# Kernel tuning notes

Hardware: AMD Instinct MI355X
Metric: run time of the kernel (lower is better)

The kernel has to match this reference:

```python
import jax, jax.numpy as jnp
import numpy as np
from jax import lax


def conv2d(x, w, b, pad):
    out = lax.conv_general_dilated(x, w, (1, 1), [(pad, pad), (pad, pad)],
                                   dimension_numbers=('NCHW', 'OIHW', 'NCHW'))
    return out + b[None, :, None, None]


def deform_conv3x3(src, offset, weight, bias):
    # torchvision.ops.deform_conv2d, 3x3 kernel, stride 1, pad 1, no mask.
    # src [B,C,H,W]; offset [B,18,H,W] laid out (y,x) per kernel pos, row-major.
    B, C, H, W = src.shape
    off = offset.reshape(B, 9, 2, H, W)
    ky, kx = jnp.meshgrid(jnp.arange(3) - 1, jnp.arange(3) - 1, indexing='ij')
    ky = ky.reshape(9).astype(src.dtype)
    kx = kx.reshape(9).astype(src.dtype)
    yy = jnp.arange(H, dtype=src.dtype)[:, None]
    xx = jnp.arange(W, dtype=src.dtype)[None, :]
    py = yy[None, None] + ky[None, :, None, None] + off[:, :, 0]  # [B,9,H,W]
    px = xx[None, None] + kx[None, :, None, None] + off[:, :, 1]
    y0 = jnp.floor(py)
    x0 = jnp.floor(px)
    wy1 = py - y0
    wx1 = px - x0

    def gather(yi, xi):
        valid = ((yi >= 0) & (yi < H) & (xi >= 0) & (xi < W)).astype(src.dtype)
        yc = jnp.clip(yi, 0, H - 1).astype(jnp.int32)
        xc = jnp.clip(xi, 0, W - 1).astype(jnp.int32)
        vals = jax.vmap(lambda s, a, c: s[:, a, c])(src, yc, xc)  # [B,C,9,H,W]
        return vals * valid[:, None]

    sampled = (gather(y0, x0) * ((1 - wy1) * (1 - wx1))[:, None]
               + gather(y0, x0 + 1) * ((1 - wy1) * wx1)[:, None]
               + gather(y0 + 1, x0) * (wy1 * (1 - wx1))[:, None]
               + gather(y0 + 1, x0 + 1) * (wy1 * wx1)[:, None])
    wk = weight.reshape(weight.shape[0], weight.shape[1], 9)
    return jnp.einsum('bckhw,ock->bohw', sampled, wk) + bias[None, :, None, None]


def setup_inputs() -> dict:
    key = jax.random.key(0)
    ks = jax.random.split(key, 16)
    B, C, H, W, N = 1, 256, 96, 96, 8
    current_feat = jax.random.normal(ks[0], (B, C, H, W), dtype=jnp.float32)
    neighbor_feats = jax.random.normal(ks[1], (N, B, C, H, W), dtype=jnp.float32)
    coord_diffs = jax.random.normal(ks[2], (N, 4), dtype=jnp.float32)
    align_w = jax.random.normal(ks[3], (C, C, 3, 3), dtype=jnp.float32) * 0.02
    align_b = jax.random.normal(ks[4], (C,), dtype=jnp.float32) * 0.02
    offset_w = jax.random.normal(ks[5], (18, 2 * C, 3, 3), dtype=jnp.float32) * 0.002
    offset_b = jax.random.normal(ks[6], (18,), dtype=jnp.float32) * 0.002
    gate1_w = jax.random.normal(ks[7], (C // 2, 2 * C, 3, 3), dtype=jnp.float32) * 0.02
    gate1_b = jax.random.normal(ks[8], (C // 2,), dtype=jnp.float32) * 0.02
    gate2_w = jax.random.normal(ks[9], (1, C // 2, 1, 1), dtype=jnp.float32) * 0.02
    gate2_b = jax.random.normal(ks[10], (1,), dtype=jnp.float32) * 0.02
    enc_w = jax.random.normal(ks[11], (C, 4), dtype=jnp.float32) * 0.1
    enc_b = jax.random.normal(ks[12], (C,), dtype=jnp.float32) * 0.1
    return dict(current_feat=current_feat, neighbor_feats=neighbor_feats,
                coord_diffs=coord_diffs, align_w=align_w, align_b=align_b,
                offset_w=offset_w, offset_b=offset_b, gate1_w=gate1_w,
                gate1_b=gate1_b, gate2_w=gate2_w, gate2_b=gate2_b,
                enc_w=enc_w, enc_b=enc_b)


def reference(current_feat, neighbor_feats, coord_diffs, align_w, align_b,
              offset_w, offset_b, gate1_w, gate1_b, gate2_w, gate2_b,
              enc_w, enc_b):
    B, C, H, W = current_feat.shape
    N = neighbor_feats.shape[0]
    aligned = []
    for n in range(N):  # fixed small neighbor set (<= 8)
        src = neighbor_feats[n]
        concat = jnp.concatenate([src, current_feat], axis=1)  # [B,2C,H,W]
        offset = conv2d(concat, offset_w, offset_b, 1)         # [B,18,H,W]
        aligned.append(deform_conv3x3(src, offset, align_w, align_b))
    all_feats = jnp.stack(aligned, axis=1)                     # [B,N,C,H,W]
    # coordinate embedding: Linear(4 -> C) per neighbor, shaped [1,N,C,1,1]
    coord_embs = (coord_diffs @ enc_w.T + enc_b)[None, :, :, None, None]
    cur_exp = jnp.broadcast_to(current_feat[:, None], (B, N, C, H, W))
    energy = jnp.concatenate([cur_exp, all_feats], axis=2).reshape(B * N, 2 * C, H, W)
    g = jax.nn.relu(conv2d(energy, gate1_w, gate1_b, 1))
    g = jax.nn.sigmoid(conv2d(g, gate2_w, gate2_b, 0))          # [B*N,1,H,W]
    weights = jax.nn.softmax(g.reshape(B, N, 1, H, W), axis=1)
    fused = (all_feats * weights + coord_embs).sum(axis=1)      # [B,C,H,W]
    return current_feat + 0.5 * fused
```

## Files before the change

### kernel.cpp

```cpp
#include <hip/hip_runtime.h>
#include <math.h>

#define CH   256
#define HH   96
#define WW   96
#define NN   8
#define HWSZ 9216
#define PLANE (HWSZ*CH)

typedef unsigned short u16;
typedef unsigned int   u32;
typedef short bf16x8 __attribute__((ext_vector_type(8)));
typedef float f32x4  __attribute__((ext_vector_type(4)));
typedef float f32x2  __attribute__((ext_vector_type(2)));

__device__ inline u16 f2bf(float f) {
    union { float f; u32 u; } v; v.f = f;
    u32 r = v.u + 0x7FFF + ((v.u >> 16) & 1);
    return (u16)(r >> 16);
}
__device__ inline float bflo(u32 u) {
    union { u32 u; float f; } v; v.u = u << 16; return v.f;
}
__device__ inline float bfhi(u32 u) {
    union { u32 u; float f; } v; v.u = u & 0xffff0000u; return v.f;
}
__device__ inline u32 pk2bf(float lo, float hi) {
    union { float f; u32 u; } a, b; a.f = lo; b.f = hi;
    u32 ra = a.u + 0x7FFF + ((a.u >> 16) & 1);
    u32 rb = b.u + 0x7FFF + ((b.u >> 16) & 1);
    return (ra >> 16) | (rb & 0xffff0000u);
}

__global__ void k_emb_sum(const float* __restrict__ cd,
                          const float* __restrict__ enc_w,
                          const float* __restrict__ enc_b,
                          float* __restrict__ emb)
{
    int c = threadIdx.x;
    float s = 0.f;
    for (int n = 0; n < NN; ++n) {
        float d = enc_b[c];
        #pragma unroll
        for (int j = 0; j < 4; ++j) d += cd[n*4 + j] * enc_w[c*4 + j];
        s += d;
    }
    emb[c] = s;
}

__global__ __launch_bounds__(256) void k_to_nhwc(const float* __restrict__ in,
                                                 u16* __restrict__ out)
{
    int n = blockIdx.y;
    int p0 = blockIdx.x * 64;
    int tid = threadIdx.x;
    __shared__ u16 T[64][262];

    int px4 = (tid & 15) * 4, cb = tid >> 4;
    for (int it = 0; it < 16; ++it) {
        int c = cb + it*16;
        float4 v = *reinterpret_cast<const float4*>(
            in + ((size_t)n*CH + c)*HWSZ + p0 + px4);
        T[px4+0][c] = f2bf(v.x);
        T[px4+1][c] = f2bf(v.y);
        T[px4+2][c] = f2bf(v.z);
        T[px4+3][c] = f2bf(v.w);
    }
    __syncthreads();
    int pxb = tid >> 5, ck = tid & 31;
    for (int it = 0; it < 8; ++it) {
        int p = pxb + it*8;
        *reinterpret_cast<int4*>(out + (size_t)n*PLANE + (size_t)(p0+p)*CH + ck*8) =
            *reinterpret_cast<const int4*>(&T[p][ck*8]);
    }
}

__global__ void k_pack_w(const float* __restrict__ w, u16* __restrict__ wp,
                         int O, int O_pad, int CIN)
{
    int idx = blockIdx.x * 256 + threadIdx.x;
    int total = O_pad * CIN * 9;
    if (idx >= total) return;
    int o = idx / (CIN * 9);
    int K = idx % (CIN * 9);
    int tap = K / CIN, c = K % CIN;
    float v = (o < O) ? w[((size_t)o * CIN + c) * 9 + tap] : 0.f;
    int NKC = (CIN * 9) >> 5;
    int kc = K >> 5, kl = K & 31;
    int lane = (kl >> 3) * 16 + (o & 15);
    size_t dstp = (((size_t)(o >> 4) * NKC + kc) * 64 + lane) * 8 + (kl & 7);
    wp[dstp] = f2bf(v);
}

template<int MTW, int EPI>
__global__ __launch_bounds__(512) void k_conv_nhwc(
    const u16* __restrict__ in0, long s0,
    const u16* __restrict__ in1, long s1,
    const u16* __restrict__ Wp, const float* __restrict__ b1,
    const float* __restrict__ g2w, const float* __restrict__ g2b,
    float* __restrict__ out)
{
    constexpr int NKC = 144, NCC = 16;
    int n = blockIdx.x, t = blockIdx.y;
    int tx0 = (t % 3) * 32, ty0 = (t / 3) * 8;
    int tid = threadIdx.x, lane = tid & 63, w = tid >> 6;
    int mh = w >> 2, pg = w & 3;
    int colq = lane >> 4;

    __shared__ __align__(16) u16 SB[340*40];
    __shared__ float gpart[8][64];

    f32x4 acc[MTW][4];
    #pragma unroll
    for (int mt = 0; mt < MTW; ++mt)
        #pragma unroll
        for (int nf = 0; nf < 4; ++nf)
            acc[mt][nf] = (f32x4){0.f,0.f,0.f,0.f};

    int bidx[4];
    #pragma unroll
    for (int nf = 0; nf < 4; ++nf) {
        int px = pg*64 + nf*16 + (lane & 15);
        int row = px >> 5, col = px & 31;
        bidx[nf] = ((row+1)*34 + (col+1))*40 + colq*8;
    }

    for (int cc = 0; cc < NCC; ++cc) {
        const u16* base = (cc < 8) ? in0 + (size_t)n*s0 + cc*32
                                   : in1 + (size_t)n*s1 + (cc-8)*32;
        for (int i = tid; i < 1360; i += 512) {
            int ph = i >> 2, q = i & 3;
            int r = ph / 34, col = ph - r*34;
            int y = ty0 - 1 + r, x = tx0 - 1 + col;
            bool v = ((unsigned)y < (unsigned)HH) && ((unsigned)x < (unsigned)WW);
            int off = v ? (y*WW + x)*CH : 0;
            int4 val = *reinterpret_cast<const int4*>(base + off + q*8);
            if (!v) val = make_int4(0,0,0,0);
            *reinterpret_cast<int4*>(&SB[ph*40 + q*8]) = val;
        }
        __syncthreads();
        #pragma unroll
        for (int tap = 0; tap < 9; ++tap) {
            int kc = tap*NCC + cc;
            bf16x8 a[MTW];
            #pragma unroll
            for (int mt = 0; mt < MTW; ++mt)
                a[mt] = *reinterpret_cast<const bf16x8*>(
                    Wp + (((size_t)(mh*MTW+mt)*NKC + kc)*64 + lane)*8);
            const int dy = tap/3 - 1, dx = tap%3 - 1;
            #pragma unroll
            for (int nf = 0; nf < 4; ++nf) {
                bf16x8 b = *reinterpret_cast<const bf16x8*>(
                    &SB[bidx[nf] + (dy*34 + dx)*40]);
                #pragma unroll
                for (int mt = 0; mt < MTW; ++mt)
                    acc[mt][nf] = __builtin_amdgcn_mfma_f32_16x16x32_bf16(
                                      a[mt], b, acc[mt][nf], 0, 0, 0);
            }
        }
        __syncthreads();
    }

    if (EPI == 0) {
        #pragma unroll
        for (int nf = 0; nf < 4; ++nf) {
            int px = pg*64 + nf*16 + (lane & 15);
            int gp = (ty0 + (px>>5))*WW + tx0 + (px & 31);
            #pragma unroll
            for (int mt = 0; mt < MTW; ++mt) {
                int o_base = (mh*MTW+mt)*16 + colq*4;
                #pragma unroll
                for (int r = 0; r < 4; ++r) {
                    int o = o_base + r;
                    if (o < 18)
                        out[((size_t)n*18 + o)*HWSZ + gp] = acc[mt][nf][r] + b1[o];
                }
            }
        }
    } else {
        float part[4];
        #pragma unroll
        for (int nf = 0; nf < 4; ++nf) {
            float s = 0.f;
            #pragma unroll
            for (int mt = 0; mt < MTW; ++mt) {
                int o_base = (mh*MTW+mt)*16 + colq*4;
                #pragma unroll
                for (int r = 0; r < 4; ++r) {
                    int o = o_base + r;
                    float vv = fmaxf(acc[mt][nf][r] + b1[o], 0.f);
                    s += vv * g2w[o];
                }
            }
            part[nf] = s;
        }
        #pragma unroll
        for (int nf = 0; nf < 4; ++nf) {
            part[nf] += __shfl_xor(part[nf], 16, 64);
            part[nf] += __shfl_xor(part[nf], 32, 64);
        }
        if (lane < 16) {
            #pragma unroll
            for (int nf = 0; nf < 4; ++nf)
                gpart[w][nf*16 + lane] = part[nf];
        }
        __syncthreads();
        if (tid < 256) {
            int pxl = tid & 63, pgg = tid >> 6;
            float s = gpart[pgg][pxl] + gpart[4 + pgg][pxl] + g2b[0];
            float g = 1.f / (1.f + expf(-s));
            int px = pgg*64 + pxl;
            int gp = (ty0 + (px>>5))*WW + tx0 + (px & 31);
            out[(size_t)n*HWSZ + gp] = g;
        }
    }
}

__global__ __launch_bounds__(256) void k_deform_nhwc(
    const u16* __restrict__ nbrh, const float* __restrict__ offs,
    const u16* __restrict__ Wp, const float* __restrict__ ab,
    u16* __restrict__ alig)
{
    constexpr int NKC = 72;
    int n = blockIdx.x, t = blockIdx.y;
    int tx0 = (t % 3) * 32, ty0 = (t / 3) * 2;
    int tid = threadIdx.x, lane = tid & 63, w = tid >> 6;
    int colq = lane >> 4;

    __shared__ __align__(16) char pool[26624];
    u16*    SB0  = (u16*)pool;
    u16*    SB1  = SB0 + 2048;
    int4*   cofs = (int4*)(pool + 8192);
    float4* cwt  = (float4*)(pool + 17408);

    const u16* src = nbrh + (size_t)n * PLANE;

    for (int i = tid; i < 576; i += 256) {
        int tt = i >> 6, p = i & 63;
        int y = ty0 + (p>>5), x = tx0 + (p & 31);
        int pp = y*WW + x;
        float oy = offs[((size_t)n*18 + 2*tt    )*HWSZ + pp];
        float ox = offs[((size_t)n*18 + 2*tt + 1)*HWSZ + pp];
        float py  = (float)y + (float)(tt/3 - 1) + oy;
        float pxx = (float)x + (float)(tt%3 - 1) + ox;
        py  = fminf(fmaxf(py,  -4.f), 100.f);
        pxx = fminf(fmaxf(pxx, -4.f), 100.f);
        float y0f = floorf(py), x0f = floorf(pxx);
        int y0 = (int)y0f, x0 = (int)x0f;
        float wy = py - y0f, wx = pxx - x0f;
        bool b00 = (y0 >= 0)  & (y0 < HH)   & (x0 >= 0)  & (x0 < WW);
        bool b01 = (y0 >= 0)  & (y0 < HH)   & (x0 >= -1) & (x0 < WW-1);
        bool b10 = (y0 >= -1) & (y0 < HH-1) & (x0 >= 0)  & (x0 < WW);
        bool b11 = (y0 >= -1) & (y0 < HH-1) & (x0 >= -1) & (x0 < WW-1);
        int a00 = (y0*WW + x0)*CH;
        int4 o4;
        o4.x = b00 ? a00             : 0;
        o4.y = b01 ? a00 + CH        : 0;
        o4.z = b10 ? a00 + WW*CH     : 0;
        o4.w = b11 ? a00 + WW*CH+CH  : 0;
        float4 w4;
        w4.x = b00 ? (1.f-wy)*(1.f-wx) : 0.f;
        w4.y = b01 ? (1.f-wy)*wx       : 0.f;
        w4.z = b10 ? wy*(1.f-wx)       : 0.f;
        w4.w = b11 ? wy*wx             : 0.f;
        cofs[i] = o4; cwt[i] = w4;
    }
    __syncthreads();

    f32x4 acc[4][4];
    #pragma unroll
    for (int mt = 0; mt < 4; ++mt)
        #pragma unroll
        for (int nf = 0; nf < 4; ++nf)
            acc[mt][nf] = (f32x4){0.f,0.f,0.f,0.f};

    int sbw = ((lane>>4)*4 + w)*128 + (lane&15)*8;
    int bb[4];
    #pragma unroll
    for (int nf = 0; nf < 4; ++nf)
        bb[nf] = (nf*4 + colq)*128 + (lane&15)*8;

    int4 o4; float4 w4;
    int4 crn[4];
    bf16x8 apf[4];

    auto loadC = [&](int kc) {
        int c0 = (kc & 7)*32 + w*8;
        crn[0] = *reinterpret_cast<const int4*>(src + o4.x + c0);
        crn[1] = *reinterpret_cast<const int4*>(src + o4.y + c0);
        crn[2] = *reinterpret_cast<const int4*>(src + o4.z + c0);
        crn[3] = *reinterpret_cast<const int4*>(src + o4.w + c0);
    };
    auto loadA = [&](int kc) {
        #pragma unroll
        for (int mt = 0; mt < 4; ++mt)
            apf[mt] = *reinterpret_cast<const bf16x8*>(
                Wp + (((size_t)(w*4+mt)*NKC + kc)*64 + lane)*8);
    };
    auto bilerp = [&](float4 wt, const int4* q) -> int4 {
        f32x2 W00 = {wt.x, wt.x}, W01 = {wt.y, wt.y};
        f32x2 W10 = {wt.z, wt.z}, W11 = {wt.w, wt.w};
        int4 res;
        #pragma unroll
        for (int j = 0; j < 4; ++j) {
            u32 u00 = ((const u32*)&q[0])[j], u01 = ((const u32*)&q[1])[j];
            u32 u10 = ((const u32*)&q[2])[j], u11 = ((const u32*)&q[3])[j];
            f32x2 c00 = {bflo(u00), bfhi(u00)};
            f32x2 c01 = {bflo(u01), bfhi(u01)};
            f32x2 c10 = {bflo(u10), bfhi(u10)};
            f32x2 c11 = {bflo(u11), bfhi(u11)};
            f32x2 v = c00*W00;
            v += c01*W01;
            v += c10*W10;
            v += c11*W11;
            ((u32*)&res)[j] = pk2bf(v.x, v.y);
        }
        return res;
    };

    o4 = cofs[lane]; w4 = cwt[lane];
    loadC(0);
    loadA(0);
    int cur = 0;
    for (int kc = 0; kc < NKC; ++kc) {
        int4 vpk = bilerp(w4, crn);
        u16* SBc = cur ? SB1 : SB0;
        *reinterpret_cast<int4*>(&SBc[sbw]) = vpk;
        bf16x8 a4[4];
        #pragma unroll
        for (int mt = 0; mt < 4; ++mt) a4[mt] = apf[mt];
        int kn = kc + 1;
        if (kn < NKC) {
            if ((kn & 7) == 0) {
                int r = (kn >> 3)*64 + lane;
                o4 = cofs[r]; w4 = cwt[r];
            }
            loadC(kn);
            loadA(kn);
        }
        __syncthreads();
        #pragma unroll
        for (int nf = 0; nf < 4; ++nf) {
            bf16x8 b = *reinterpret_cast<const bf16x8*>(&SBc[bb[nf]]);
            #pragma unroll
            for (int mt = 0; mt < 4; ++mt)
                acc[mt][nf] = __builtin_amdgcn_mfma_f32_16x16x32_bf16(
                                  a4[mt], b, acc[mt][nf], 0, 0, 0);
        }
        cur ^= 1;
    }

    __syncthreads();
    u16* TO = (u16*)pool;
    u16* aligp = alig + (size_t)n * PLANE;
    #pragma unroll
    for (int h = 0; h < 2; ++h) {
        #pragma unroll
        for (int sub = 0; sub < 2; ++sub) {
            int nf = 2*h + sub;
            int pl = sub*16 + (lane & 15);
            #pragma unroll
            for (int mt = 0; mt < 4; ++mt) {
                int o = (w*4+mt)*16 + colq*4;
                ushort4 v;
                v.x = f2bf(acc[mt][nf][0] + ab[o]);
                v.y = f2bf(acc[mt][nf][1] + ab[o+1]);
                v.z = f2bf(acc[mt][nf][2] + ab[o+2]);
                v.w = f2bf(acc[mt][nf][3] + ab[o+3]);
                *reinterpret_cast<ushort4*>(&TO[pl*264 + o]) = v;
            }
        }
        __syncthreads();
        #pragma unroll
        for (int it = 0; it < 4; ++it) {
            int i = tid + it*256;
            int pr = i >> 5, ck = i & 31;
            int nf = 2*h + (pr >> 4);
            int pxx = nf*16 + (pr & 15);
            int gp = (ty0 + (pxx>>5))*WW + tx0 + (pxx & 31);
            *reinterpret_cast<int4*>(aligp + (size_t)gp*CH + ck*8) =
                *reinterpret_cast<const int4*>(&TO[pr*264 + ck*8]);
        }
        __syncthreads();
    }
}

__global__ __launch_bounds__(256) void k_fuse_nhwc(
    const float* __restrict__ cur, const u16* __restrict__ alig,
    const float* __restrict__ g, const float* __restrict__ emb,
    float* __restrict__ out)
{
    int p0 = blockIdx.x * 32;
    int tid = threadIdx.x;
    __shared__ float wE[NN][32];
    __shared__ float trans[256][33];

    if (tid < 32) {
        int p = p0 + tid;
        float e[NN], m = -1e30f;
        #pragma unroll
        for (int n = 0; n < NN; ++n) { e[n] = g[n*HWSZ + p]; m = fmaxf(m, e[n]); }
        float se = 0.f;
        #pragma unroll
        for (int n = 0; n < NN; ++n) { e[n] = expf(e[n] - m); se += e[n]; }
        float inv = 1.f / se;
        #pragma unroll
        for (int n = 0; n < NN; ++n) wE[n][tid] = e[n] * inv;
    }
    __syncthreads();

    #pragma unroll
    for (int it = 0; it < 4; ++it) {
        int i = tid + it*256;
        int px = i >> 5, ck = i & 31;
        float a8[8];
        #pragma unroll
        for (int j = 0; j < 8; ++j) a8[j] = 0.f;
        #pragma unroll
        for (int n = 0; n < NN; ++n) {
            int4 v = *reinterpret_cast<const int4*>(
                &alig[((size_t)n*HWSZ + p0 + px)*CH + ck*8]);
            float f = wE[n][px];
            #pragma unroll
            for (int j4 = 0; j4 < 4; ++j4) {
                u32 u = ((const u32*)&v)[j4];
                a8[2*j4]   += bflo(u) * f;
                a8[2*j4+1] += bfhi(u) * f;
            }
        }
        #pragma unroll
        for (int j = 0; j < 8; ++j) {
            int c = ck*8 + j;
            trans[c][px ^ (c & 31)] = a8[j] + emb[c];
        }
    }
    __syncthreads();
    for (int it = 0; it < 32; ++it) {
        int c = (tid >> 5) + it*8, px = tid & 31;
        int idx = c*HWSZ + p0 + px;
        out[idx] = cur[idx] + 0.5f * trans[c][px ^ (c & 31)];
    }
}

extern "C" void kernel_launch(void* const* d_in, const int* in_sizes, int n_in,
                              void* d_out, int out_size, void* d_ws, size_t ws_size,
                              hipStream_t stream)
{
    const float* cur = (const float*)d_in[0];
    const float* nbr = (const float*)d_in[1];
    const float* cd  = (const float*)d_in[2];
    const float* aw  = (const float*)d_in[3];
    const float* ab  = (const float*)d_in[4];
    const float* ow  = (const float*)d_in[5];
    const float* ob  = (const float*)d_in[6];
    const float* g1w = (const float*)d_in[7];
    const float* g1b = (const float*)d_in[8];
    const float* g2w = (const float*)d_in[9];
    const float* g2b = (const float*)d_in[10];
    const float* ew  = (const float*)d_in[11];
    const float* eb  = (const float*)d_in[12];
    float* out = (float*)d_out;
    float* ws  = (float*)d_ws;

    float* offs = ws;
    float* gbuf = offs + 1327104;
    float* emb  = gbuf + 73728;
    u16* nbrh = (u16*)(emb + 256);
    u16* curh = nbrh + (size_t)NN*PLANE;
    u16* alig = curh + PLANE;
    u16* wpO  = alig + (size_t)NN*PLANE;
    u16* wpG  = wpO + 147456;
    u16* wpA  = wpG + 589824;

    k_emb_sum<<<dim3(1), dim3(256), 0, stream>>>(cd, ew, eb, emb);
    k_to_nhwc<<<dim3(144, 8), dim3(256), 0, stream>>>(nbr, nbrh);
    k_to_nhwc<<<dim3(144, 1), dim3(256), 0, stream>>>(cur, curh);
    k_pack_w<<<dim3((32*4608 + 255)/256), dim3(256), 0, stream>>>(ow, wpO, 18, 32, 512);
    k_pack_w<<<dim3((128*4608 + 255)/256), dim3(256), 0, stream>>>(g1w, wpG, 128, 128, 512);
    k_pack_w<<<dim3((256*2304 + 255)/256), dim3(256), 0, stream>>>(aw, wpA, 256, 256, 256);

    k_conv_nhwc<1, 0><<<dim3(8, 36), dim3(512), 0, stream>>>(
        nbrh, (long)PLANE, curh, 0L, wpO, ob, nullptr, nullptr, offs);
    k_deform_nhwc<<<dim3(8, 144), dim3(256), 0, stream>>>(nbrh, offs, wpA, ab, alig);
    k_conv_nhwc<4, 1><<<dim3(8, 36), dim3(512), 0, stream>>>(
        curh, 0L, alig, (long)PLANE, wpG, g1b, g2w, g2b, gbuf);
    k_fuse_nhwc<<<dim3(288), dim3(256), 0, stream>>>(cur, alig, gbuf, emb, out);
}
```

Baseline: 435.0 us.

## Prefetch two K-chunks ahead and remap gather threads with swizzled LDS layout

```diff
diff --git a/kernel.cpp b/kernel.cpp
--- a/kernel.cpp
+++ b/kernel.cpp
@@ -274,24 +274,30 @@
         for (int nf = 0; nf < 4; ++nf)
             acc[mt][nf] = (f32x4){0.f,0.f,0.f,0.f};
 
-    int sbw = ((lane>>4)*4 + w)*128 + (lane&15)*8;
+    int px = tid >> 2, chq = tid & 3;
+    int sbw = ((px>>4)*4 + chq)*128 + (((px&15) ^ (chq<<2)))*8;
     int bb[4];
     #pragma unroll
     for (int nf = 0; nf < 4; ++nf)
-        bb[nf] = (nf*4 + colq)*128 + (lane&15)*8;
-
-    int4 o4; float4 w4;
-    int4 crn[4];
-    bf16x8 apf[4];
-
-    auto loadC = [&](int kc) {
-        int c0 = (kc & 7)*32 + w*8;
+        bb[nf] = (nf*4 + colq)*128 + (((lane&15) ^ (colq<<2)))*8;
+    int c0base = chq*8;
+
+    int4 o4_0, o4_1; float4 w4_0, w4_1;
+    int4 crn0[4], crn1[4];
+    bf16x8 apf0[4], apf1[4];
+
+    auto loadCoord = [&](int kc, int4& o4, float4& w4) {
+        int r = (kc >> 3)*64 + px;
+        o4 = cofs[r]; w4 = cwt[r];
+    };
+    auto loadC = [&](int kc, const int4& o4, int4* crn) {
+        int c0 = (kc & 7)*32 + c0base;
         crn[0] = *reinterpret_cast<const int4*>(src + o4.x + c0);
         crn[1] = *reinterpret_cast<const int4*>(src + o4.y + c0);
         crn[2] = *reinterpret_cast<const int4*>(src + o4.z + c0);
         crn[3] = *reinterpret_cast<const int4*>(src + o4.w + c0);
     };
-    auto loadA = [&](int kc) {
+    auto loadA = [&](int kc, bf16x8* apf) {
         #pragma unroll
         for (int mt = 0; mt < 4; ++mt)
             apf[mt] = *reinterpret_cast<const bf16x8*>(
@@ -318,25 +324,19 @@
         return res;
     };
 
-    o4 = cofs[lane]; w4 = cwt[lane];
-    loadC(0);
-    loadA(0);
     int cur = 0;
-    for (int kc = 0; kc < NKC; ++kc) {
+    auto step = [&](int kc, int4& o4, float4& w4, int4* crn, bf16x8* apf) {
         int4 vpk = bilerp(w4, crn);
         u16* SBc = cur ? SB1 : SB0;
         *reinterpret_cast<int4*>(&SBc[sbw]) = vpk;
         bf16x8 a4[4];
         #pragma unroll
         for (int mt = 0; mt < 4; ++mt) a4[mt] = apf[mt];
-        int kn = kc + 1;
+        int kn = kc + 2;
         if (kn < NKC) {
-            if ((kn & 7) == 0) {
-                int r = (kn >> 3)*64 + lane;
-                o4 = cofs[r]; w4 = cwt[r];
-            }
-            loadC(kn);
-            loadA(kn);
+            if ((kn & 7) < 2) loadCoord(kn, o4, w4);
+            loadC(kn, o4, crn);
+            loadA(kn, apf);
         }
         __syncthreads();
         #pragma unroll
@@ -348,6 +348,16 @@
                                   a4[mt], b, acc[mt][nf], 0, 0, 0);
         }
         cur ^= 1;
+    };
+
+    loadCoord(0, o4_0, w4_0);
+    loadCoord(1, o4_1, w4_1);
+    loadC(0, o4_0, crn0); loadA(0, apf0);
+    loadC(1, o4_1, crn1); loadA(1, apf1);
+
+    for (int kc = 0; kc < NKC; kc += 2) {
+        step(kc,     o4_0, w4_0, crn0, apf0);
+        step(kc + 1, o4_1, w4_1, crn1, apf1);
     }
 
     __syncthreads();
```

New measurement: 406.8 us. 6.5% less time.

## Warp-specialize deform conv into bilinear producer and MFMA consumer waves

Applied to the files above, without the earlier changes.

```diff
diff --git a/kernel.cpp b/kernel.cpp
--- a/kernel.cpp
+++ b/kernel.cpp
@@ -216,7 +216,7 @@
     }
 }
 
-__global__ __launch_bounds__(256) void k_deform_nhwc(
+__global__ __launch_bounds__(512, 4) void k_deform_nhwc(
     const u16* __restrict__ nbrh, const float* __restrict__ offs,
     const u16* __restrict__ Wp, const float* __restrict__ ab,
     u16* __restrict__ alig)
@@ -227,15 +227,15 @@
     int tid = threadIdx.x, lane = tid & 63, w = tid >> 6;
     int colq = lane >> 4;
 
-    __shared__ __align__(16) char pool[26624];
+    __shared__ __align__(16) char pool[29696];
     u16*    SB0  = (u16*)pool;
-    u16*    SB1  = SB0 + 2048;
-    int4*   cofs = (int4*)(pool + 8192);
-    float4* cwt  = (float4*)(pool + 17408);
+    u16*    SB1  = SB0 + 2816;
+    int4*   cofs = (int4*)(pool + 11264);
+    float4* cwt  = (float4*)(pool + 20480);
 
     const u16* src = nbrh + (size_t)n * PLANE;
 
-    for (int i = tid; i < 576; i += 256) {
+    for (int i = tid; i < 576; i += 512) {
         int tt = i >> 6, p = i & 63;
         int y = ty0 + (p>>5), x = tx0 + (p & 31);
         int pp = y*WW + x;
@@ -274,106 +274,130 @@
         for (int nf = 0; nf < 4; ++nf)
             acc[mt][nf] = (f32x4){0.f,0.f,0.f,0.f};
 
-    int sbw = ((lane>>4)*4 + w)*128 + (lane&15)*8;
-    int bb[4];
-    #pragma unroll
-    for (int nf = 0; nf < 4; ++nf)
-        bb[nf] = (nf*4 + colq)*128 + (lane&15)*8;
-
-    int4 o4; float4 w4;
-    int4 crn[4];
-    bf16x8 apf[4];
-
-    auto loadC = [&](int kc) {
-        int c0 = (kc & 7)*32 + w*8;
-        crn[0] = *reinterpret_cast<const int4*>(src + o4.x + c0);
-        crn[1] = *reinterpret_cast<const int4*>(src + o4.y + c0);
-        crn[2] = *reinterpret_cast<const int4*>(src + o4.z + c0);
-        crn[3] = *reinterpret_cast<const int4*>(src + o4.w + c0);
-    };
-    auto loadA = [&](int kc) {
-        #pragma unroll
-        for (int mt = 0; mt < 4; ++mt)
-            apf[mt] = *reinterpret_cast<const bf16x8*>(
-                Wp + (((size_t)(w*4+mt)*NKC + kc)*64 + lane)*8);
-    };
-    auto bilerp = [&](float4 wt, const int4* q) -> int4 {
-        f32x2 W00 = {wt.x, wt.x}, W01 = {wt.y, wt.y};
-        f32x2 W10 = {wt.z, wt.z}, W11 = {wt.w, wt.w};
-        int4 res;
-        #pragma unroll
-        for (int j = 0; j < 4; ++j) {
-            u32 u00 = ((const u32*)&q[0])[j], u01 = ((const u32*)&q[1])[j];
-            u32 u10 = ((const u32*)&q[2])[j], u11 = ((const u32*)&q[3])[j];
-            f32x2 c00 = {bflo(u00), bfhi(u00)};
-            f32x2 c01 = {bflo(u01), bfhi(u01)};
-            f32x2 c10 = {bflo(u10), bfhi(u10)};
-            f32x2 c11 = {bflo(u11), bfhi(u11)};
-            f32x2 v = c00*W00;
-            v += c01*W01;
-            v += c10*W10;
-            v += c11*W11;
-            ((u32*)&res)[j] = pk2bf(v.x, v.y);
-        }
-        return res;
-    };
-
-    o4 = cofs[lane]; w4 = cwt[lane];
-    loadC(0);
-    loadA(0);
-    int cur = 0;
-    for (int kc = 0; kc < NKC; ++kc) {
-        int4 vpk = bilerp(w4, crn);
-        u16* SBc = cur ? SB1 : SB0;
-        *reinterpret_cast<int4*>(&SBc[sbw]) = vpk;
-        bf16x8 a4[4];
-        #pragma unroll
-        for (int mt = 0; mt < 4; ++mt) a4[mt] = apf[mt];
-        int kn = kc + 1;
-        if (kn < NKC) {
-            if ((kn & 7) == 0) {
-                int r = (kn >> 3)*64 + lane;
-                o4 = cofs[r]; w4 = cwt[r];
-            }
-            loadC(kn);
-            loadA(kn);
-        }
-        __syncthreads();
-        #pragma unroll
-        for (int nf = 0; nf < 4; ++nf) {
-            bf16x8 b = *reinterpret_cast<const bf16x8*>(&SBc[bb[nf]]);
+    if (w < 4) {
+        int px = tid >> 2, chq = tid & 3;
+        int sbw = px*44 + chq*8;
+        int cb  = chq*8;
+        int4 crn0[4], crn1[4];
+
+        auto loadC = [&](int kp, int4* crn) {
+            int4 o4 = cofs[(kp >> 3)*64 + px];
+            int c0 = (kp & 7)*32 + cb;
+            crn[0] = *reinterpret_cast<const int4*>(src + o4.x + c0);
+            crn[1] = *reinterpret_cast<const int4*>(src + o4.y + c0);
+            crn[2] = *reinterpret_cast<const int4*>(src + o4.z + c0);
+            crn[3] = *reinterpret_cast<const int4*>(src + o4.w + c0);
+        };
+        auto produce = [&](int kp, const int4* q, u16* SBc) {
+            float4 wt = cwt[(kp >> 3)*64 + px];
+            f32x2 W00 = {wt.x, wt.x}, W01 = {wt.y, wt.y};
+            f32x2 W10 = {wt.z, wt.z}, W11 = {wt.w, wt.w};
+            int4 res;
+            #pragma unroll
+            for (int j = 0; j < 4; ++j) {
+                u32 u00 = ((const u32*)&q[0])[j], u01 = ((const u32*)&q[1])[j];
+                u32 u10 = ((const u32*)&q[2])[j], u11 = ((const u32*)&q[3])[j];
+                f32x2 c00 = {bflo(u00), bfhi(u00)};
+                f32x2 c01 = {bflo(u01), bfhi(u01)};
+                f32x2 c10 = {bflo(u10), bfhi(u10)};
+                f32x2 c11 = {bflo(u11), bfhi(u11)};
+                f32x2 v = c00*W00;
+                v += c01*W01;
+                v += c10*W10;
+                v += c11*W11;
+                ((u32*)&res)[j] = pk2bf(v.x, v.y);
+            }
+            *reinterpret_cast<int4*>(&SBc[sbw]) = res;
+        };
+
+        loadC(0, crn0);
+        loadC(1, crn1);
+        produce(0, crn0, SB0);
+        loadC(2, crn0);
+        __syncthreads();
+
+        for (int kc = 0; kc < NKC; kc += 2) {
+            produce(kc + 1, crn1, SB1);
+            if (kc + 3 < NKC) loadC(kc + 3, crn1);
+            __syncthreads();
+            if (kc + 2 < NKC) {
+                produce(kc + 2, crn0, SB0);
+                if (kc + 4 < NKC) loadC(kc + 4, crn0);
+            }
+            __syncthreads();
+        }
+    } else {
+        int wc = w - 4;
+        int bb[4];
+        #pragma unroll
+        for (int nf = 0; nf < 4; ++nf)
+            bb[nf] = (nf*16 + (lane & 15))*44 + colq*8;
+
+        bf16x8 apfA[4], apfB[4];
+        auto loadA = [&](int kc, bf16x8* apf) {
             #pragma unroll
             for (int mt = 0; mt < 4; ++mt)
-                acc[mt][nf] = __builtin_amdgcn_mfma_f32_16x16x32_bf16(
-                                  a4[mt], b, acc[mt][nf], 0, 0, 0);
-        }
-        cur ^= 1;
-    }
-
-    __syncthreads();
+                apf[mt] = *reinterpret_cast<const bf16x8*>(
+                    Wp + (((size_t)(wc*4+mt)*NKC + kc)*64 + lane)*8);
+        };
+        loadA(0, apfA);
+        loadA(1, apfB);
+        __syncthreads();
+
+        for (int kc = 0; kc < NKC; kc += 2) {
+            __builtin_amdgcn_s_setprio(1);
+            #pragma unroll
+            for (int nf = 0; nf < 4; ++nf) {
+                bf16x8 b = *reinterpret_cast<const bf16x8*>(&SB0[bb[nf]]);
+                #pragma unroll
+                for (int mt = 0; mt < 4; ++mt)
+                    acc[mt][nf] = __builtin_amdgcn_mfma_f32_16x16x32_bf16(
+                                      apfA[mt], b, acc[mt][nf], 0, 0, 0);
+            }
+            __builtin_amdgcn_s_setprio(0);
+            if (kc + 2 < NKC) loadA(kc + 2, apfA);
+            __syncthreads();
+            __builtin_amdgcn_s_setprio(1);
+            #pragma unroll
+            for (int nf = 0; nf < 4; ++nf) {
+                bf16x8 b = *reinterpret_cast<const bf16x8*>(&SB1[bb[nf]]);
+                #pragma unroll
+                for (int mt = 0; mt < 4; ++mt)
+                    acc[mt][nf] = __builtin_amdgcn_mfma_f32_16x16x32_bf16(
+                                      apfB[mt], b, acc[mt][nf], 0, 0, 0);
+            }
+            __builtin_amdgcn_s_setprio(0);
+            if (kc + 3 < NKC) loadA(kc + 3, apfB);
+            __syncthreads();
+        }
+    }
+
     u16* TO = (u16*)pool;
     u16* aligp = alig + (size_t)n * PLANE;
     #pragma unroll
     for (int h = 0; h < 2; ++h) {
-        #pragma unroll
-        for (int sub = 0; sub < 2; ++sub) {
-            int nf = 2*h + sub;
-            int pl = sub*16 + (lane & 15);
-            #pragma unroll
-            for (int mt = 0; mt < 4; ++mt) {
-                int o = (w*4+mt)*16 + colq*4;
-                ushort4 v;
-                v.x = f2bf(acc[mt][nf][0] + ab[o]);
-                v.y = f2bf(acc[mt][nf][1] + ab[o+1]);
-                v.z = f2bf(acc[mt][nf][2] + ab[o+2]);
-                v.w = f2bf(acc[mt][nf][3] + ab[o+3]);
-                *reinterpret_cast<ushort4*>(&TO[pl*264 + o]) = v;
-            }
-        }
-        __syncthreads();
-        #pragma unroll
-        for (int it = 0; it < 4; ++it) {
-            int i = tid + it*256;
+        if (w >= 4) {
+            int wc = w - 4;
+            #pragma unroll
+            for (int sub = 0; sub < 2; ++sub) {
+                int nf = 2*h + sub;
+                int pl = sub*16 + (lane & 15);
+                #pragma unroll
+                for (int mt = 0; mt < 4; ++mt) {
+                    int o = (wc*4+mt)*16 + colq*4;
+                    ushort4 v;
+                    v.x = f2bf(acc[mt][nf][0] + ab[o]);
+                    v.y = f2bf(acc[mt][nf][1] + ab[o+1]);
+                    v.z = f2bf(acc[mt][nf][2] + ab[o+2]);
+                    v.w = f2bf(acc[mt][nf][3] + ab[o+3]);
+                    *reinterpret_cast<ushort4*>(&TO[pl*264 + o]) = v;
+                }
+            }
+        }
+        __syncthreads();
+        #pragma unroll
+        for (int it = 0; it < 2; ++it) {
+            int i = tid + it*512;
             int pr = i >> 5, ck = i & 31;
             int nf = 2*h + (pr >> 4);
             int pxx = nf*16 + (pr & 15);
@@ -481,7 +505,7 @@
 
     k_conv_nhwc<1, 0><<<dim3(8, 36), dim3(512), 0, stream>>>(
         nbrh, (long)PLANE, curh, 0L, wpO, ob, nullptr, nullptr, offs);
-    k_deform_nhwc<<<dim3(8, 144), dim3(256), 0, stream>>>(nbrh, offs, wpA, ab, alig);
+    k_deform_nhwc<<<dim3(8, 144), dim3(512), 0, stream>>>(nbrh, offs, wpA, ab, alig);
     k_conv_nhwc<4, 1><<<dim3(8, 36), dim3(512), 0, stream>>>(
         curh, 0L, alig, (long)PLANE, wpG, g1b, g2w, g2b, gbuf);
     k_fuse_nhwc<<<dim3(288), dim3(256), 0, stream>>>(cur, alig, gbuf, emb, out);
```

After: 456.1 us. 1.05x slower.

## Stage a haloed source window in LDS for deformable-conv bilinear sampling

Applied to the files above, without the earlier changes.

```diff
diff --git a/kernel.cpp b/kernel.cpp
--- a/kernel.cpp
+++ b/kernel.cpp
@@ -76,7 +76,7 @@
 }
 
 __global__ void k_pack_w(const float* __restrict__ w, u16* __restrict__ wp,
-                         int O, int O_pad, int CIN)
+                         int O, int O_pad, int CIN, int order)
 {
     int idx = blockIdx.x * 256 + threadIdx.x;
     int total = O_pad * CIN * 9;
@@ -86,7 +86,8 @@
     int tap = K / CIN, c = K % CIN;
     float v = (o < O) ? w[((size_t)o * CIN + c) * 9 + tap] : 0.f;
     int NKC = (CIN * 9) >> 5;
-    int kc = K >> 5, kl = K & 31;
+    int kc = order ? ((c >> 5)*9 + tap) : (tap*(CIN >> 5) + (c >> 5));
+    int kl = c & 31;
     int lane = (kl >> 3) * 16 + (o & 15);
     size_t dstp = (((size_t)(o >> 4) * NKC + kc) * 64 + lane) * 8 + (kl & 7);
     wp[dstp] = f2bf(v);
@@ -227,11 +228,12 @@
     int tid = threadIdx.x, lane = tid & 63, w = tid >> 6;
     int colq = lane >> 4;
 
-    __shared__ __align__(16) char pool[26624];
-    u16*    SB0  = (u16*)pool;
-    u16*    SB1  = SB0 + 2048;
-    int4*   cofs = (int4*)(pool + 8192);
-    float4* cwt  = (float4*)(pool + 17408);
+    __shared__ __align__(16) char pool[50944];
+    u16*    LW   = (u16*)pool;
+    u16*    SB0  = (u16*)(pool + 28160);
+    u16*    SB1  = (u16*)(pool + 33792);
+    float4* cwt  = (float4*)(pool + 39424);
+    int*    widx = (int*)(pool + 48640);
 
     const u16* src = nbrh + (size_t)n * PLANE;
 
@@ -252,18 +254,14 @@
         bool b01 = (y0 >= 0)  & (y0 < HH)   & (x0 >= -1) & (x0 < WW-1);
         bool b10 = (y0 >= -1) & (y0 < HH-1) & (x0 >= 0)  & (x0 < WW);
         bool b11 = (y0 >= -1) & (y0 < HH-1) & (x0 >= -1) & (x0 < WW-1);
-        int a00 = (y0*WW + x0)*CH;
-        int4 o4;
-        o4.x = b00 ? a00             : 0;
-        o4.y = b01 ? a00 + CH        : 0;
-        o4.z = b10 ? a00 + WW*CH     : 0;
-        o4.w = b11 ? a00 + WW*CH+CH  : 0;
         float4 w4;
         w4.x = b00 ? (1.f-wy)*(1.f-wx) : 0.f;
         w4.y = b01 ? (1.f-wy)*wx       : 0.f;
         w4.z = b10 ? wy*(1.f-wx)       : 0.f;
         w4.w = b11 ? wy*wx             : 0.f;
-        cofs[i] = o4; cwt[i] = w4;
+        cwt[i] = w4;
+        bool inw = (y0 >= ty0-3) & (y0 <= ty0+3) & (x0 >= tx0-3) & (x0 <= tx0+35);
+        widx[i] = inw ? ((y0-(ty0-3))*40 + (x0-(tx0-3)))*44 : -1;
     }
     __syncthreads();
 
@@ -274,37 +272,59 @@
         for (int nf = 0; nf < 4; ++nf)
             acc[mt][nf] = (f32x4){0.f,0.f,0.f,0.f};
 
-    int sbw = ((lane>>4)*4 + w)*128 + (lane&15)*8;
+    int px = tid >> 2, chq = tid & 3;
+    int sbw = px*44 + chq*8;
     int bb[4];
     #pragma unroll
     for (int nf = 0; nf < 4; ++nf)
-        bb[nf] = (nf*4 + colq)*128 + (lane&15)*8;
-
-    int4 o4; float4 w4;
-    int4 crn[4];
+        bb[nf] = (nf*16 + (lane & 15))*44 + colq*8;
+
     bf16x8 apf[4];
-
-    auto loadC = [&](int kc) {
-        int c0 = (kc & 7)*32 + w*8;
-        crn[0] = *reinterpret_cast<const int4*>(src + o4.x + c0);
-        crn[1] = *reinterpret_cast<const int4*>(src + o4.y + c0);
-        crn[2] = *reinterpret_cast<const int4*>(src + o4.z + c0);
-        crn[3] = *reinterpret_cast<const int4*>(src + o4.w + c0);
-    };
     auto loadA = [&](int kc) {
         #pragma unroll
         for (int mt = 0; mt < 4; ++mt)
             apf[mt] = *reinterpret_cast<const bf16x8*>(
                 Wp + (((size_t)(w*4+mt)*NKC + kc)*64 + lane)*8);
     };
-    auto bilerp = [&](float4 wt, const int4* q) -> int4 {
+
+    auto produce = [&](int tap, int cc, u16* SBc) {
+        int r = (tap << 6) + px;
+        int bi = widx[r];
+        float4 wt = cwt[r];
+        int4 q0, q1, q2, q3;
+        if (bi >= 0) {
+            int base = bi + chq*8;
+            q0 = *reinterpret_cast<const int4*>(&LW[base]);
+            q1 = *reinterpret_cast<const int4*>(&LW[base + 44]);
+            q2 = *reinterpret_cast<const int4*>(&LW[base + 1760]);
+            q3 = *reinterpret_cast<const int4*>(&LW[base + 1804]);
+        } else {
+            int y = ty0 + (px>>5), x = tx0 + (px & 31);
+            int pp = y*WW + x;
+            float oy = offs[((size_t)n*18 + 2*tap    )*HWSZ + pp];
+            float ox = offs[((size_t)n*18 + 2*tap + 1)*HWSZ + pp];
+            float py  = (float)y + (float)(tap/3 - 1) + oy;
+            float pxx = (float)x + (float)(tap%3 - 1) + ox;
+            py  = fminf(fmaxf(py,  -4.f), 100.f);
+            pxx = fminf(fmaxf(pxx, -4.f), 100.f);
+            int y0 = (int)floorf(py), x0 = (int)floorf(pxx);
+            bool b00 = (y0 >= 0)  & (y0 < HH)   & (x0 >= 0)  & (x0 < WW);
+            bool b01 = (y0 >= 0)  & (y0 < HH)   & (x0 >= -1) & (x0 < WW-1);
+            bool b10 = (y0 >= -1) & (y0 < HH-1) & (x0 >= 0)  & (x0 < WW);
+            bool b11 = (y0 >= -1) & (y0 < HH-1) & (x0 >= -1) & (x0 < WW-1);
+            int a00 = (y0*WW + x0)*CH + cc*32 + chq*8;
+            q0 = *reinterpret_cast<const int4*>(src + (b00 ? a00            : 0));
+            q1 = *reinterpret_cast<const int4*>(src + (b01 ? a00 + CH       : 0));
+            q2 = *reinterpret_cast<const int4*>(src + (b10 ? a00 + WW*CH    : 0));
+            q3 = *reinterpret_cast<const int4*>(src + (b11 ? a00 + WW*CH+CH : 0));
+        }
         f32x2 W00 = {wt.x, wt.x}, W01 = {wt.y, wt.y};
         f32x2 W10 = {wt.z, wt.z}, W11 = {wt.w, wt.w};
         int4 res;
         #pragma unroll
         for (int j = 0; j < 4; ++j) {
-            u32 u00 = ((const u32*)&q[0])[j], u01 = ((const u32*)&q[1])[j];
-            u32 u10 = ((const u32*)&q[2])[j], u11 = ((const u32*)&q[3])[j];
+            u32 u00 = ((const u32*)&q0)[j], u01 = ((const u32*)&q1)[j];
+            u32 u10 = ((const u32*)&q2)[j], u11 = ((const u32*)&q3)[j];
             f32x2 c00 = {bflo(u00), bfhi(u00)};
             f32x2 c01 = {bflo(u01), bfhi(u01)};
             f32x2 c10 = {bflo(u10), bfhi(u10)};
@@ -315,42 +335,42 @@
             v += c11*W11;
             ((u32*)&res)[j] = pk2bf(v.x, v.y);
         }
-        return res;
+        *reinterpret_cast<int4*>(&SBc[sbw]) = res;
     };
 
-    o4 = cofs[lane]; w4 = cwt[lane];
-    loadC(0);
-    loadA(0);
     int cur = 0;
-    for (int kc = 0; kc < NKC; ++kc) {
-        int4 vpk = bilerp(w4, crn);
-        u16* SBc = cur ? SB1 : SB0;
-        *reinterpret_cast<int4*>(&SBc[sbw]) = vpk;
-        bf16x8 a4[4];
-        #pragma unroll
-        for (int mt = 0; mt < 4; ++mt) a4[mt] = apf[mt];
-        int kn = kc + 1;
-        if (kn < NKC) {
-            if ((kn & 7) == 0) {
-                int r = (kn >> 3)*64 + lane;
-                o4 = cofs[r]; w4 = cwt[r];
+    for (int cc = 0; cc < 8; ++cc) {
+        for (int u = tid; u < 1280; u += 256) {
+            int wp = u >> 2, q = u & 3;
+            int row = wp / 40, col = wp - row*40;
+            int y = ty0 - 3 + row, x = tx0 - 3 + col;
+            bool v = ((unsigned)y < (unsigned)HH) && ((unsigned)x < (unsigned)WW);
+            int4 val = v ? *reinterpret_cast<const int4*>(
+                               src + (y*WW + x)*CH + cc*32 + q*8)
+                         : make_int4(0,0,0,0);
+            *reinterpret_cast<int4*>(&LW[(row*40+col)*44 + q*8]) = val;
+        }
+        __syncthreads();
+        #pragma unroll
+        for (int tap = 0; tap < 9; ++tap) {
+            int kc = cc*9 + tap;
+            loadA(kc);
+            produce(tap, cc, cur ? SB1 : SB0);
+            __syncthreads();
+            u16* SBc = cur ? SB1 : SB0;
+            #pragma unroll
+            for (int nf = 0; nf < 4; ++nf) {
+                bf16x8 b = *reinterpret_cast<const bf16x8*>(&SBc[bb[nf]]);
+                #pragma unroll
+                for (int mt = 0; mt < 4; ++mt)
+                    acc[mt][nf] = __builtin_amdgcn_mfma_f32_16x16x32_bf16(
+                                      apf[mt], b, acc[mt][nf], 0, 0, 0);
             }
-            loadC(kn);
-            loadA(kn);
-        }
-        __syncthreads();
-        #pragma unroll
-        for (int nf = 0; nf < 4; ++nf) {
-            bf16x8 b = *reinterpret_cast<const bf16x8*>(&SBc[bb[nf]]);
-            #pragma unroll
-            for (int mt = 0; mt < 4; ++mt)
-                acc[mt][nf] = __builtin_amdgcn_mfma_f32_16x16x32_bf16(
-                                  a4[mt], b, acc[mt][nf], 0, 0, 0);
-        }
-        cur ^= 1;
-    }
-
-    __syncthreads();
+            cur ^= 1;
+        }
+        __syncthreads();
+    }
+
     u16* TO = (u16*)pool;
     u16* aligp = alig + (size_t)n * PLANE;
     #pragma unroll
@@ -475,9 +495,9 @@
     k_emb_sum<<<dim3(1), dim3(256), 0, stream>>>(cd, ew, eb, emb);
     k_to_nhwc<<<dim3(144, 8), dim3(256), 0, stream>>>(nbr, nbrh);
     k_to_nhwc<<<dim3(144, 1), dim3(256), 0, stream>>>(cur, curh);
-    k_pack_w<<<dim3((32*4608 + 255)/256), dim3(256), 0, stream>>>(ow, wpO, 18, 32, 512);
-    k_pack_w<<<dim3((128*4608 + 255)/256), dim3(256), 0, stream>>>(g1w, wpG, 128, 128, 512);
-    k_pack_w<<<dim3((256*2304 + 255)/256), dim3(256), 0, stream>>>(aw, wpA, 256, 256, 256);
+    k_pack_w<<<dim3((32*4608 + 255)/256), dim3(256), 0, stream>>>(ow, wpO, 18, 32, 512, 0);
+    k_pack_w<<<dim3((128*4608 + 255)/256), dim3(256), 0, stream>>>(g1w, wpG, 128, 128, 512, 0);
+    k_pack_w<<<dim3((256*2304 + 255)/256), dim3(256), 0, stream>>>(aw, wpA, 256, 256, 256, 1);
 
     k_conv_nhwc<1, 0><<<dim3(8, 36), dim3(512), 0, stream>>>(
         nbrh, (long)PLANE, curh, 0L, wpO, ob, nullptr, nullptr, offs);
```

Result: slower. 668.3 us (+53.6%).
